# Kernel optimization log

Measured on AMD Instinct MI355X. Metric: run time of the kernel, lower is better.

## Reference

```python
import jax, jax.numpy as jnp
import numpy as np

N_EMBD = 1024
N_HEAD = 16
B, T = 2, 2048
LN_EPS = 1e-5


def _linear_params(key, d_in, d_out):
    k1, k2 = jax.random.split(key)
    bound = 1.0 / np.sqrt(d_in)
    W = jax.random.uniform(k1, (d_in, d_out), jnp.float32, -bound, bound)
    b = jax.random.uniform(k2, (d_out,), jnp.float32, -bound, bound)
    return W, b


def setup_inputs() -> dict:
    key = jax.random.key(0)
    ks = jax.random.split(key, 8)
    x = jax.random.normal(ks[0], (B, T, N_EMBD), jnp.float32)
    Wq, bq = _linear_params(ks[1], N_EMBD, N_EMBD)
    Wk, bk = _linear_params(ks[2], N_EMBD, N_EMBD)
    Wv, bv = _linear_params(ks[3], N_EMBD, N_EMBD)
    Wo, bo = _linear_params(ks[4], N_EMBD, N_EMBD)
    W1, b1 = _linear_params(ks[5], N_EMBD, 4 * N_EMBD)
    W2, b2 = _linear_params(ks[6], 4 * N_EMBD, N_EMBD)
    ln1_g = jnp.ones((N_EMBD,), jnp.float32)
    ln1_b = jnp.zeros((N_EMBD,), jnp.float32)
    ln2_g = jnp.ones((N_EMBD,), jnp.float32)
    ln2_b = jnp.zeros((N_EMBD,), jnp.float32)
    return dict(x=x, Wq=Wq, bq=bq, Wk=Wk, bk=bk, Wv=Wv, bv=bv, Wo=Wo, bo=bo,
                W1=W1, b1=b1, W2=W2, b2=b2,
                ln1_g=ln1_g, ln1_b=ln1_b, ln2_g=ln2_g, ln2_b=ln2_b)


def _layernorm(x, g, b):
    mu = jnp.mean(x, axis=-1, keepdims=True)
    var = jnp.mean(jnp.square(x - mu), axis=-1, keepdims=True)
    return (x - mu) * jax.lax.rsqrt(var + LN_EPS) * g + b


def _attention(x, Wq, bq, Wk, bk, Wv, bv, Wo, bo):
    Bsz, Tlen, C = x.shape
    hd = C // N_HEAD
    q = (x @ Wq + bq).reshape(Bsz, Tlen, N_HEAD, hd)
    k = (x @ Wk + bk).reshape(Bsz, Tlen, N_HEAD, hd)
    v = (x @ Wv + bv).reshape(Bsz, Tlen, N_HEAD, hd)
    scale = 1.0 / np.sqrt(hd)
    # NOTE: the original module's mask buffer is all ones -> masked_fill is a
    # no-op, so attention is FULL (non-causal) despite the class name.
    att = jnp.einsum('bqhd,bkhd->bhqk', q, k) * scale
    att = jax.nn.softmax(att, axis=-1)
    y = jnp.einsum('bhqk,bkhd->bqhd', att, v).reshape(Bsz, Tlen, C)
    return y @ Wo + bo


def reference(x, Wq, bq, Wk, bk, Wv, bv, Wo, bo, W1, b1, W2, b2,
              ln1_g, ln1_b, ln2_g, ln2_b):
    x = x + _attention(_layernorm(x, ln1_g, ln1_b), Wq, bq, Wk, bk, Wv, bv, Wo, bo)
    h = _layernorm(x, ln2_g, ln2_b)
    h = jax.nn.gelu(h @ W1 + b1, approximate=False) @ W2 + b2
    return x + h
```

## Files before the change

kernel.cpp:

```cpp
#include <hip/hip_runtime.h>
#include <hip/hip_bf16.h>
#include <math.h>


typedef __bf16 bf16x8 __attribute__((ext_vector_type(8)));
typedef float f32x4 __attribute__((ext_vector_type(4)));

__device__ __forceinline__ unsigned short f2bf(float f) {
  union { float f; unsigned int u; } v; v.f = f;
  unsigned int u = v.u;
  unsigned int r = (u + 0x7fffu + ((u >> 16) & 1u)) >> 16;
  return (unsigned short)r;
}

__device__ __forceinline__ unsigned int fbits(float f) {
  union { float f; unsigned int u; } v; v.f = f;
  return v.u;
}

__device__ __forceinline__ bf16x8 ld_bf16x8(const unsigned short* p) {
  union { uint4 u; bf16x8 v; } x;
  x.u = *(const uint4*)p;
  return x.v;
}

__device__ __forceinline__ float fast_exp2(float x) {
#if __has_builtin(__builtin_amdgcn_exp2f)
  return __builtin_amdgcn_exp2f(x);
#else
  return exp2f(x);
#endif
}

__device__ __forceinline__ size_t ckidx(int row, int col, int Kd) {
  return ((size_t)(row >> 4) * (Kd >> 5) + (col >> 5)) * 512 +
         (size_t)(((col >> 3) & 3) * 128 + (row & 15) * 8 + (col & 7));
}

__device__ __forceinline__ void async_copy16(const void* g, void* l) {
  __builtin_amdgcn_global_load_lds(
      (const __attribute__((address_space(1))) void*)g,
      (__attribute__((address_space(3))) void*)l, 16, 0, 0);
}

__global__ __launch_bounds__(256) void prep_kernel(
    const float* __restrict__ Wq, const float* __restrict__ Wk,
    const float* __restrict__ Wv, const float* __restrict__ Wo,
    const float* __restrict__ W1, const float* __restrict__ W2,
    unsigned short* __restrict__ WqT, unsigned short* __restrict__ WkT,
    unsigned short* __restrict__ WvT, unsigned short* __restrict__ WoT,
    unsigned short* __restrict__ W1T, unsigned short* __restrict__ W2T,
    const float* __restrict__ x, const float* __restrict__ g,
    const float* __restrict__ b, unsigned short* __restrict__ xn) {
  __shared__ unsigned short tile[32][33];
  __shared__ float red[8];
  const int id = blockIdx.x;
  const int t = threadIdx.x;

  if (id < 12288) {
    const float* W;
    unsigned short* Wt;
    int N, K, bx, by;
    if (id < 4096) {
      const int wsel = id >> 10, b10 = id & 1023;
      W = wsel == 0 ? Wq : (wsel == 1 ? Wk : (wsel == 2 ? Wv : Wo));
      Wt = wsel == 0 ? WqT : (wsel == 1 ? WkT : (wsel == 2 ? WvT : WoT));
      N = 1024; K = 1024; bx = b10 & 31; by = b10 >> 5;
    } else if (id < 8192) {
      const int b12 = id - 4096;
      W = W1; Wt = W1T; N = 4096; K = 1024; bx = b12 & 127; by = b12 >> 7;
    } else {
      const int b12 = id - 8192;
      W = W2; Wt = W2T; N = 1024; K = 4096; bx = b12 & 31; by = b12 >> 5;
    }
    const int n0 = bx * 32, k0 = by * 32;
    const int r = t >> 3, cq = (t & 7) * 4;
    float4 v = *(const float4*)&W[(size_t)(k0 + r) * N + n0 + cq];
    tile[cq + 0][r] = f2bf(v.x);
    tile[cq + 1][r] = f2bf(v.y);
    tile[cq + 2][r] = f2bf(v.z);
    tile[cq + 3][r] = f2bf(v.w);
    __syncthreads();
    ushort4 o;
    o.x = tile[r][cq + 0];
    o.y = tile[r][cq + 1];
    o.z = tile[r][cq + 2];
    o.w = tile[r][cq + 3];
    *(ushort4*)&Wt[ckidx(n0 + r, k0 + cq, K)] = o;
  } else {
    const int row = id - 12288;
    const float4 v = ((const float4*)(x + (size_t)row * 1024))[t];
    float s = v.x + v.y + v.z + v.w;
    float s2 = v.x * v.x + v.y * v.y + v.z * v.z + v.w * v.w;
    for (int o = 32; o > 0; o >>= 1) {
      s += __shfl_xor(s, o, 64);
      s2 += __shfl_xor(s2, o, 64);
    }
    const int w = t >> 6;
    if ((t & 63) == 0) { red[w] = s; red[4 + w] = s2; }
    __syncthreads();
    s = red[0] + red[1] + red[2] + red[3];
    s2 = red[4] + red[5] + red[6] + red[7];
    const float mu = s * (1.f / 1024.f);
    const float var = s2 * (1.f / 1024.f) - mu * mu;
    const float rs = rsqrtf(var + 1e-5f);
    const float4 gg = ((const float4*)g)[t];
    const float4 bb = ((const float4*)b)[t];
    ushort4 o4;
    o4.x = f2bf((v.x - mu) * rs * gg.x + bb.x);
    o4.y = f2bf((v.y - mu) * rs * gg.y + bb.y);
    o4.z = f2bf((v.z - mu) * rs * gg.z + bb.z);
    o4.w = f2bf((v.w - mu) * rs * gg.w + bb.w);
    *(ushort4*)&xn[ckidx(row, t * 4, 1024)] = o4;
  }
}

__global__ __launch_bounds__(256) void ln_kernel(
    const float* __restrict__ x, const float* __restrict__ g,
    const float* __restrict__ b, unsigned short* __restrict__ out) {
  const int row = blockIdx.x, t = threadIdx.x;
  const float4 v = ((const float4*)(x + (size_t)row * 1024))[t];
  float s = v.x + v.y + v.z + v.w;
  float s2 = v.x * v.x + v.y * v.y + v.z * v.z + v.w * v.w;
  for (int o = 32; o > 0; o >>= 1) {
    s += __shfl_xor(s, o, 64);
    s2 += __shfl_xor(s2, o, 64);
  }
  __shared__ float red[8];
  const int w = t >> 6;
  if ((t & 63) == 0) { red[w] = s; red[4 + w] = s2; }
  __syncthreads();
  s = red[0] + red[1] + red[2] + red[3];
  s2 = red[4] + red[5] + red[6] + red[7];
  const float mu = s * (1.f / 1024.f);
  const float var = s2 * (1.f / 1024.f) - mu * mu;
  const float rs = rsqrtf(var + 1e-5f);
  const float4 gg = ((const float4*)g)[t];
  const float4 bb = ((const float4*)b)[t];
  ushort4 o4;
  o4.x = f2bf((v.x - mu) * rs * gg.x + bb.x);
  o4.y = f2bf((v.y - mu) * rs * gg.y + bb.y);
  o4.z = f2bf((v.z - mu) * rs * gg.z + bb.z);
  o4.w = f2bf((v.w - mu) * rs * gg.w + bb.w);
  *(ushort4*)&out[ckidx(row, t * 4, 1024)] = o4;
}

enum { MODE_QKV = 0, MODE_RES = 1, MODE_GELU = 2 };

#define QSCALE 0.18033688011112043f

template <int MODE>
__global__ __launch_bounds__(512) void gemm256_kernel(
    const unsigned short* __restrict__ A, const unsigned short* __restrict__ Bt,
    const float* __restrict__ bias0, const float* __restrict__ bias1,
    const float* __restrict__ bias2,
    void* __restrict__ out0, void* __restrict__ out1, void* __restrict__ out2,
    int M, int N, int K) {
  __shared__ __align__(16) unsigned short L[2][64 * 512];
  const int t = threadIdx.x;
  const int l = t & 63, w = t >> 6;
  const int l8 = l * 8;
  const int lr = l & 15, lq = l >> 4;

  const int NT = N >> 8;
  const int q8 = (int)gridDim.x >> 3;
  const int bid = blockIdx.x;
  const int wg = (bid & 7) * q8 + (bid >> 3);
  const int mt = wg / NT, nt = wg % NT;
  const int m0 = mt << 8, n0 = nt << 8;

  const int ag0 = (w >> 2) * 8;
  const int bg0 = (w & 3) * 4;
  const int K32 = K >> 5;

  f32x4 acc[8][4];
#pragma unroll
  for (int i = 0; i < 8; i++)
#pragma unroll
    for (int j = 0; j < 4; j++) {
      f32x4 z = {0.f, 0.f, 0.f, 0.f};
      acc[i][j] = z;
    }

  auto issue = [&](int kt, int slot) {
    const int k32 = kt * 2;
#pragma unroll
    for (int j = 0; j < 8; j++) {
      const int c = j * 8 + w;
      unsigned short* dst = &L[slot][c * 512 + l8];
      if (j < 4) {
        const size_t cid =
            (size_t)((m0 >> 4) + (c & 15)) * K32 + (k32 + (c >> 4));
        async_copy16(&A[cid * 512 + l8], dst);
      } else {
        const int cb = c - 32;
        const size_t cid =
            (size_t)((n0 >> 4) + (cb & 15)) * K32 + (k32 + (cb >> 4));
        async_copy16(&Bt[cid * 512 + l8], dst);
      }
    }
  };

  const int KT = K >> 6;
  issue(0, 0);
  for (int kt = 0; kt < KT; kt++) {
    const int slot = kt & 1;
    if (kt + 1 < KT) {
      issue(kt + 1, slot ^ 1);
      asm volatile("s_waitcnt vmcnt(8)" ::: "memory");
    } else {
      asm volatile("s_waitcnt vmcnt(0)" ::: "memory");
    }
    __builtin_amdgcn_s_barrier();

    bf16x8 bfr[2][4];
#pragma unroll
    for (int kk = 0; kk < 2; kk++)
#pragma unroll
      for (int nj = 0; nj < 4; nj++)
        bfr[kk][nj] =
            ld_bf16x8(&L[slot][(32 + kk * 16 + bg0 + nj) * 512 + l8]);

#pragma unroll
    for (int half = 0; half < 2; half++) {
#pragma unroll
      for (int kk = 0; kk < 2; kk++) {
        bf16x8 afr[4];
#pragma unroll
        for (int mi = 0; mi < 4; mi++)
          afr[mi] = ld_bf16x8(
              &L[slot][(kk * 16 + ag0 + half * 4 + mi) * 512 + l8]);
        __builtin_amdgcn_s_setprio(1);
#pragma unroll
        for (int mi = 0; mi < 4; mi++)
#pragma unroll
          for (int nj = 0; nj < 4; nj++)
            acc[half * 4 + mi][nj] = __builtin_amdgcn_mfma_f32_16x16x32_bf16(
                afr[mi], bfr[kk][nj], acc[half * 4 + mi][nj], 0, 0, 0);
        __builtin_amdgcn_s_setprio(0);
      }
    }
    __builtin_amdgcn_s_barrier();
  }

#pragma unroll
  for (int mi8 = 0; mi8 < 8; mi8++) {
#pragma unroll
    for (int nj = 0; nj < 4; nj++) {
#pragma unroll
      for (int i = 0; i < 4; i++) {
        const int gm = m0 + (w >> 2) * 128 + mi8 * 16 + lq * 4 + i;
        const int gn = n0 + (w & 3) * 64 + nj * 16 + lr;
        const float v = acc[mi8][nj][i];
        if (MODE == MODE_QKV) {
          const int sel = gn >> 10, cn = gn & 1023;
          const int hh = cn >> 6, d = cn & 63;
          const int bb2 = gm >> 11, tok = gm & 2047;
          const size_t bh = (size_t)bb2 * 16 + hh;
          float u = v + (sel == 0 ? bias0 : (sel == 1 ? bias1 : bias2))[cn];
          if (sel == 0) {
            u *= QSCALE;
            const int qt = tok >> 7, r7 = tok & 127;
            const int ww = r7 >> 5, ss = (r7 >> 4) & 1, qlr = r7 & 15;
            const int kk = d >> 5, lq2 = (d >> 3) & 3, e = d & 7;
            const size_t idx =
                (((((bh * 16 + qt) * 4 + ww) * 2 + ss) * 2 + kk) << 9) +
                (lq2 * 16 + qlr) * 8 + e;
            ((unsigned short*)out0)[idx] = f2bf(u);
          } else if (sel == 1) {
            const int ktile = tok >> 6, r6 = tok & 63;
            const int nt2 = r6 >> 4, klr = r6 & 15;
            const int kk = d >> 5, lq2 = (d >> 3) & 3, e = d & 7;
            const size_t idx =
                ((((bh * 32 + ktile) * 4 + nt2) * 2 + kk) << 9) +
                (lq2 * 16 + klr) * 8 + e;
            ((unsigned short*)out1)[idx] = f2bf(u);
          } else {
            const int ktile = tok >> 6, r6 = tok & 63;
            const int kb = r6 >> 5, lq2 = (r6 >> 3) & 3, e = r6 & 7;
            const int nt2 = d >> 4, vlr = d & 15;
            const size_t idx =
                ((((bh * 32 + ktile) * 2 + kb) * 4 + nt2) << 9) +
                (lq2 * 16 + vlr) * 8 + e;
            ((unsigned short*)out2)[idx] = f2bf(u);
          }
        } else {
          const float u = v + bias0[gn];
          const float ge = 0.5f * u * (1.f + erff(u * 0.70710678118654752f));
          ((unsigned short*)out0)[ckidx(gm, gn, N)] = f2bf(ge);
        }
      }
    }
  }
}

template <int BM, int BN, int MODE>
__global__ __launch_bounds__(256) void gemm_kernel(
    const unsigned short* __restrict__ A, const unsigned short* __restrict__ Bt,
    const float* __restrict__ bias0, const float* __restrict__ residual,
    void* __restrict__ out0, int M, int N, int K) {
  constexpr int MI = BM / 32;
  constexpr int NI = BN / 32;
  constexpr int ACH = BM / 8;
  constexpr int BCH = BN / 8;
  __shared__ __align__(16) unsigned short As[2][BM * 64];
  __shared__ __align__(16) unsigned short Bs[2][BN * 64];
  const int t = threadIdx.x;

  const int NT = N / BN;
  const int NTX = NT >> 3;
  const int bid = blockIdx.x;
  const int xcd = bid & 7, local = bid >> 3;
  const int nt_ = xcd * NTX + local % NTX;
  const int mt = local / NTX;
  const int m0 = mt * BM, n0 = nt_ * BN;

  const int l = t & 63, w = t >> 6;
  const int l8 = l * 8;
  const int lr = l & 15, lq = l >> 4;
  const int K32 = K >> 5;

  f32x4 acc[MI][NI];
#pragma unroll
  for (int i = 0; i < MI; i++)
#pragma unroll
    for (int j = 0; j < NI; j++) {
      f32x4 z = {0.f, 0.f, 0.f, 0.f};
      acc[i][j] = z;
    }

  auto issue = [&](int k0, int p) {
    const int k32 = k0 >> 5;
#pragma unroll
    for (int j = 0; j < ACH / 4; j++) {
      const int c = j * 4 + w;
      const int g = c % (BM / 16), kk = c / (BM / 16);
      const size_t cid = (size_t)((m0 >> 4) + g) * K32 + (k32 + kk);
      async_copy16(&A[cid * 512 + l8], &As[p][c * 512 + l8]);
    }
#pragma unroll
    for (int j = 0; j < BCH / 4; j++) {
      const int c = j * 4 + w;
      const int g = c % (BN / 16), kk = c / (BN / 16);
      const size_t cid = (size_t)((n0 >> 4) + g) * K32 + (k32 + kk);
      async_copy16(&Bt[cid * 512 + l8], &Bs[p][c * 512 + l8]);
    }
  };

  issue(0, 0);
  int p = 0;
  for (int k0 = 0; k0 < K; k0 += 64) {
    __syncthreads();
    if (k0 + 64 < K) issue(k0 + 64, p ^ 1);
#pragma unroll
    for (int kk = 0; kk < 2; kk++) {
      bf16x8 af[MI], bf[NI];
#pragma unroll
      for (int mi = 0; mi < MI; mi++)
        af[mi] = ld_bf16x8(
            &As[p][(kk * (BM / 16) + (w >> 1) * (BM / 32) + mi) * 512 + l8]);
#pragma unroll
      for (int ni = 0; ni < NI; ni++)
        bf[ni] = ld_bf16x8(
            &Bs[p][(kk * (BN / 16) + (w & 1) * (BN / 32) + ni) * 512 + l8]);
#pragma unroll
      for (int mi = 0; mi < MI; mi++)
#pragma unroll
        for (int ni = 0; ni < NI; ni++)
          acc[mi][ni] = __builtin_amdgcn_mfma_f32_16x16x32_bf16(
              af[mi], bf[ni], acc[mi][ni], 0, 0, 0);
    }
    p ^= 1;
  }

  const int wm = (w >> 1) * (BM / 2), wn = (w & 1) * (BN / 2);
#pragma unroll
  for (int mi = 0; mi < MI; mi++) {
#pragma unroll
    for (int ni = 0; ni < NI; ni++) {
#pragma unroll
      for (int i = 0; i < 4; i++) {
        const int gm = m0 + wm + mi * 16 + lq * 4 + i;
        const int gn = n0 + wn + ni * 16 + lr;
        ((float*)out0)[(size_t)gm * N + gn] =
            acc[mi][ni][i] + bias0[gn] + residual[(size_t)gm * N + gn];
      }
    }
  }
}

__global__ __launch_bounds__(256) void attn_kernel(
    const unsigned short* __restrict__ Qp, const unsigned short* __restrict__ Kp,
    const unsigned short* __restrict__ Vp, unsigned short* __restrict__ O) {
  __shared__ __align__(16) unsigned short Ps[128 * 72];
  const int id = blockIdx.x;
  const int xcd = id & 7, loc = id >> 3;
  const int bh = xcd * 4 + (loc >> 4);
  const int qt = loc & 15;
  const int t = threadIdx.x, l = t & 63, w = t >> 6;
  const int lr = l & 15, lq = l >> 4;
  const int l8 = l * 8;
  const size_t rowBase = (size_t)(bh >> 4) * 2048;
  const int col0 = (bh & 15) * 64;

  const unsigned short* Qb_ = Qp + ((((size_t)bh * 16 + qt) * 4 + w) << 11);
  bf16x8 qf[2][2];
#pragma unroll
  for (int s = 0; s < 2; s++)
#pragma unroll
    for (int kk = 0; kk < 2; kk++)
      qf[s][kk] = ld_bf16x8(&Qb_[((s * 2 + kk) << 9) + l8]);

  const unsigned short* Kb_ = Kp + ((size_t)bh << 17);
  const unsigned short* Vb_ = Vp + ((size_t)bh << 17);

  bf16x8 kf[2][4];
#pragma unroll
  for (int nt = 0; nt < 4; nt++)
#pragma unroll
    for (int kk = 0; kk < 2; kk++)
      kf[kk][nt] = ld_bf16x8(&Kb_[((nt * 2 + kk) << 9) + l8]);

  f32x4 oacc[2][4];
#pragma unroll
  for (int s = 0; s < 2; s++)
#pragma unroll
    for (int nt = 0; nt < 4; nt++) {
      f32x4 z = {0.f, 0.f, 0.f, 0.f};
      oacc[s][nt] = z;
    }
  float lp[2] = {0.f, 0.f};

  for (int kt = 0; kt < 32; kt++) {
    const unsigned short* vtile = Vb_ + ((size_t)kt << 12);
    bf16x8 vf[2][4];
#pragma unroll
    for (int kb = 0; kb < 2; kb++)
#pragma unroll
      for (int nt = 0; nt < 4; nt++)
        vf[kb][nt] = ld_bf16x8(&vtile[((kb * 4 + nt) << 9) + l8]);

    f32x4 st[2][4];
#pragma unroll
    for (int s = 0; s < 2; s++)
#pragma unroll
      for (int nt = 0; nt < 4; nt++) {
        f32x4 z = {0.f, 0.f, 0.f, 0.f};
        st[s][nt] = z;
      }
#pragma unroll
    for (int nt = 0; nt < 4; nt++) {
      __builtin_amdgcn_s_setprio(1);
      st[0][nt] = __builtin_amdgcn_mfma_f32_16x16x32_bf16(kf[0][nt], qf[0][0], st[0][nt], 0, 0, 0);
      st[1][nt] = __builtin_amdgcn_mfma_f32_16x16x32_bf16(kf[0][nt], qf[1][0], st[1][nt], 0, 0, 0);
      st[0][nt] = __builtin_amdgcn_mfma_f32_16x16x32_bf16(kf[1][nt], qf[0][1], st[0][nt], 0, 0, 0);
      st[1][nt] = __builtin_amdgcn_mfma_f32_16x16x32_bf16(kf[1][nt], qf[1][1], st[1][nt], 0, 0, 0);
      __builtin_amdgcn_s_setprio(0);
    }

    const unsigned short* ktile_p = Kb_ + ((size_t)((kt + 1) & 31) << 12);
#pragma unroll
    for (int nt = 0; nt < 4; nt++)
#pragma unroll
      for (int kk = 0; kk < 2; kk++)
        kf[kk][nt] = ld_bf16x8(&ktile_p[((nt * 2 + kk) << 9) + l8]);

#pragma unroll
    for (int s = 0; s < 2; s++) {
      float rsum = 0.f;
#pragma unroll
      for (int nt = 0; nt < 4; nt++)
#pragma unroll
        for (int i = 0; i < 4; i++) {
          const float pv = fast_exp2(st[s][nt][i]);
          st[s][nt][i] = pv;
          rsum += pv;
        }
      lp[s] += rsum;
    }

#pragma unroll
    for (int s = 0; s < 2; s++)
#pragma unroll
      for (int nt = 0; nt < 4; nt++) {
        uint2 pk;
        pk.x = __builtin_amdgcn_perm(fbits(st[s][nt][1]), fbits(st[s][nt][0]), 0x07060302u);
        pk.y = __builtin_amdgcn_perm(fbits(st[s][nt][3]), fbits(st[s][nt][2]), 0x07060302u);
        *(uint2*)&Ps[(w * 32 + s * 16 + lr) * 72 + nt * 16 + lq * 4] = pk;
      }

#pragma unroll
    for (int kb = 0; kb < 2; kb++) {
      bf16x8 pf0 = ld_bf16x8(&Ps[(w * 32 + lr) * 72 + kb * 32 + lq * 8]);
      bf16x8 pf1 = ld_bf16x8(&Ps[(w * 32 + 16 + lr) * 72 + kb * 32 + lq * 8]);
      __builtin_amdgcn_s_setprio(1);
#pragma unroll
      for (int nt = 0; nt < 4; nt++) {
        oacc[0][nt] = __builtin_amdgcn_mfma_f32_16x16x32_bf16(pf0, vf[kb][nt], oacc[0][nt], 0, 0, 0);
        oacc[1][nt] = __builtin_amdgcn_mfma_f32_16x16x32_bf16(pf1, vf[kb][nt], oacc[1][nt], 0, 0, 0);
      }
      __builtin_amdgcn_s_setprio(0);
    }
  }

#pragma unroll
  for (int s = 0; s < 2; s++) {
    float li = lp[s];
    li += __shfl_xor(li, 16, 64);
    li += __shfl_xor(li, 32, 64);
    const float inv = 1.f / li;
#pragma unroll
    for (int nt = 0; nt < 4; nt++)
#pragma unroll
      for (int i = 0; i < 4; i++) {
        const int orow = (int)rowBase + qt * 128 + w * 32 + s * 16 + lq * 4 + i;
        const int ocol = col0 + nt * 16 + lr;
        O[ckidx(orow, ocol, 1024)] = f2bf(oacc[s][nt][i] * inv);
      }
  }
}

extern "C" void kernel_launch(void* const* d_in, const int* in_sizes, int n_in,
                              void* d_out, int out_size, void* d_ws, size_t ws_size,
                              hipStream_t stream) {
  const float* x    = (const float*)d_in[0];
  const float* Wq   = (const float*)d_in[1];
  const float* bq   = (const float*)d_in[2];
  const float* Wk   = (const float*)d_in[3];
  const float* bk   = (const float*)d_in[4];
  const float* Wv   = (const float*)d_in[5];
  const float* bv   = (const float*)d_in[6];
  const float* Wo   = (const float*)d_in[7];
  const float* bo   = (const float*)d_in[8];
  const float* W1   = (const float*)d_in[9];
  const float* b1   = (const float*)d_in[10];
  const float* W2   = (const float*)d_in[11];
  const float* b2   = (const float*)d_in[12];
  const float* ln1g = (const float*)d_in[13];
  const float* ln1b = (const float*)d_in[14];
  const float* ln2g = (const float*)d_in[15];
  const float* ln2b = (const float*)d_in[16];

  char* ws = (char*)d_ws;
  const size_t MB = 1024ull * 1024ull;
  unsigned short* WqT = (unsigned short*)(ws + 0 * MB);
  unsigned short* WkT = (unsigned short*)(ws + 2 * MB);
  unsigned short* WvT = (unsigned short*)(ws + 4 * MB);
  unsigned short* WoT = (unsigned short*)(ws + 6 * MB);
  unsigned short* W1T = (unsigned short*)(ws + 8 * MB);
  unsigned short* W2T = (unsigned short*)(ws + 16 * MB);
  unsigned short* xn  = (unsigned short*)(ws + 24 * MB);
  unsigned short* Qp  = (unsigned short*)(ws + 32 * MB);
  unsigned short* Kp  = (unsigned short*)(ws + 40 * MB);
  unsigned short* Vp  = (unsigned short*)(ws + 48 * MB);
  unsigned short* Ob  = (unsigned short*)(ws + 56 * MB);
  float*          x1  = (float*)(ws + 64 * MB);
  unsigned short* h2  = (unsigned short*)(ws + 80 * MB);
  unsigned short* Hb  = (unsigned short*)(ws + 24 * MB);

  const dim3 blk(256);
  const dim3 blk512(512);

  prep_kernel<<<dim3(16384), blk, 0, stream>>>(
      Wq, Wk, Wv, Wo, W1, W2, WqT, WkT, WvT, WoT, W1T, W2T,
      x, ln1g, ln1b, xn);

  gemm256_kernel<MODE_QKV><<<dim3(192), blk512, 0, stream>>>(
      xn, WqT, bq, bk, bv, Qp, Kp, Vp, 4096, 3072, 1024);

  attn_kernel<<<dim3(512), blk, 0, stream>>>(Qp, Kp, Vp, Ob);

  gemm_kernel<64, 128, MODE_RES><<<dim3(8 * 64), blk, 0, stream>>>(
      Ob, WoT, bo, x, x1, 4096, 1024, 1024);

  ln_kernel<<<4096, blk, 0, stream>>>(x1, ln2g, ln2b, h2);

  gemm256_kernel<MODE_GELU><<<dim3(256), blk512, 0, stream>>>(
      h2, W1T, b1, nullptr, nullptr, Hb, nullptr, nullptr, 4096, 4096, 1024);

  gemm_kernel<64, 128, MODE_RES><<<dim3(8 * 64), blk, 0, stream>>>(
      Hb, W2T, b2, x1, (float*)d_out, 4096, 1024, 4096);
}
```

Baseline: 365.1 us.

## Replace 64x128 residual GEMM with 128x128 tile, 512-thread pipelined kernel

The templated 64x128/256-thread residual GEMM used for the output projection and the second MLP matmul is replaced by a dedicated 128x128 tile kernel with 8 waves. Each wave now computes a 64x32 sub-tile. A single shared buffer is double-buffered and synchronised with explicit vmcnt waits and raw barriers, so loads for the next tile overlap compute. MFMA sections are wrapped in raised wave priority. Larger tiles improve data reuse but halve the grid to 256 blocks, which may lower occupancy on a 256-CU device.

```diff
diff --git a/kernel.cpp b/kernel.cpp
--- a/kernel.cpp
+++ b/kernel.cpp
@@ -294,96 +294,103 @@
   }
 }
 
-template <int BM, int BN, int MODE>
-__global__ __launch_bounds__(256) void gemm_kernel(
+__global__ __launch_bounds__(512) void gemm128_kernel(
     const unsigned short* __restrict__ A, const unsigned short* __restrict__ Bt,
     const float* __restrict__ bias0, const float* __restrict__ residual,
-    void* __restrict__ out0, int M, int N, int K) {
-  constexpr int MI = BM / 32;
-  constexpr int NI = BN / 32;
-  constexpr int ACH = BM / 8;
-  constexpr int BCH = BN / 8;
-  __shared__ __align__(16) unsigned short As[2][BM * 64];
-  __shared__ __align__(16) unsigned short Bs[2][BN * 64];
+    float* __restrict__ out0, int M, int N, int K) {
+  __shared__ __align__(16) unsigned short L[2][32 * 512];
   const int t = threadIdx.x;
-
-  const int NT = N / BN;
-  const int NTX = NT >> 3;
-  const int bid = blockIdx.x;
-  const int xcd = bid & 7, local = bid >> 3;
-  const int nt_ = xcd * NTX + local % NTX;
-  const int mt = local / NTX;
-  const int m0 = mt * BM, n0 = nt_ * BN;
-
   const int l = t & 63, w = t >> 6;
   const int l8 = l * 8;
   const int lr = l & 15, lq = l >> 4;
+
+  const int NT = N >> 7;
+  const int q8 = (int)gridDim.x >> 3;
+  const int bid = blockIdx.x;
+  const int wg = (bid & 7) * q8 + (bid >> 3);
+  const int mt = wg / NT, nt = wg % NT;
+  const int m0 = mt << 7, n0 = nt << 7;
+
+  const int ag0 = (w >> 2) * 4;
+  const int bg0 = (w & 3) * 2;
   const int K32 = K >> 5;
 
-  f32x4 acc[MI][NI];
-#pragma unroll
-  for (int i = 0; i < MI; i++)
-#pragma unroll
-    for (int j = 0; j < NI; j++) {
+  f32x4 acc[4][2];
+#pragma unroll
+  for (int i = 0; i < 4; i++)
+#pragma unroll
+    for (int j = 0; j < 2; j++) {
       f32x4 z = {0.f, 0.f, 0.f, 0.f};
       acc[i][j] = z;
     }
 
-  auto issue = [&](int k0, int p) {
-    const int k32 = k0 >> 5;
-#pragma unroll
-    for (int j = 0; j < ACH / 4; j++) {
-      const int c = j * 4 + w;
-      const int g = c % (BM / 16), kk = c / (BM / 16);
-      const size_t cid = (size_t)((m0 >> 4) + g) * K32 + (k32 + kk);
-      async_copy16(&A[cid * 512 + l8], &As[p][c * 512 + l8]);
-    }
-#pragma unroll
-    for (int j = 0; j < BCH / 4; j++) {
-      const int c = j * 4 + w;
-      const int g = c % (BN / 16), kk = c / (BN / 16);
-      const size_t cid = (size_t)((n0 >> 4) + g) * K32 + (k32 + kk);
-      async_copy16(&Bt[cid * 512 + l8], &Bs[p][c * 512 + l8]);
+  auto issue = [&](int kt, int slot) {
+    const int k32 = kt * 2;
+#pragma unroll
+    for (int j = 0; j < 4; j++) {
+      const int c = j * 8 + w;
+      unsigned short* dst = &L[slot][c * 512 + l8];
+      if (j < 2) {
+        const size_t cid =
+            (size_t)((m0 >> 4) + (c & 7)) * K32 + (k32 + (c >> 3));
+        async_copy16(&A[cid * 512 + l8], dst);
+      } else {
+        const int cb = c - 16;
+        const size_t cid =
+            (size_t)((n0 >> 4) + (cb & 7)) * K32 + (k32 + (cb >> 3));
+        async_copy16(&Bt[cid * 512 + l8], dst);
+      }
     }
   };
 
+  const int KT = K >> 6;
   issue(0, 0);
-  int p = 0;
-  for (int k0 = 0; k0 < K; k0 += 64) {
-    __syncthreads();
-    if (k0 + 64 < K) issue(k0 + 64, p ^ 1);
+  for (int kt = 0; kt < KT; kt++) {
+    const int slot = kt & 1;
+    if (kt + 1 < KT) {
+      issue(kt + 1, slot ^ 1);
+      asm volatile("s_waitcnt vmcnt(4)" ::: "memory");
+    } else {
+      asm volatile("s_waitcnt vmcnt(0)" ::: "memory");
+    }
+    __builtin_amdgcn_s_barrier();
+
+    bf16x8 bfr[2][2];
+#pragma unroll
+    for (int kk = 0; kk < 2; kk++)
+#pragma unroll
+      for (int nj = 0; nj < 2; nj++)
+        bfr[kk][nj] =
+            ld_bf16x8(&L[slot][(16 + kk * 8 + bg0 + nj) * 512 + l8]);
+
 #pragma unroll
     for (int kk = 0; kk < 2; kk++) {
-      bf16x8 af[MI], bf[NI];
-#pragma unroll
-      for (int mi = 0; mi < MI; mi++)
-        af[mi] = ld_bf16x8(
-            &As[p][(kk * (BM / 16) + (w >> 1) * (BM / 32) + mi) * 512 + l8]);
-#pragma unroll
-      for (int ni = 0; ni < NI; ni++)
-        bf[ni] = ld_bf16x8(
-            &Bs[p][(kk * (BN / 16) + (w & 1) * (BN / 32) + ni) * 512 + l8]);
-#pragma unroll
-      for (int mi = 0; mi < MI; mi++)
-#pragma unroll
-        for (int ni = 0; ni < NI; ni++)
-          acc[mi][ni] = __builtin_amdgcn_mfma_f32_16x16x32_bf16(
-              af[mi], bf[ni], acc[mi][ni], 0, 0, 0);
-    }
-    p ^= 1;
-  }
-
-  const int wm = (w >> 1) * (BM / 2), wn = (w & 1) * (BN / 2);
-#pragma unroll
-  for (int mi = 0; mi < MI; mi++) {
-#pragma unroll
-    for (int ni = 0; ni < NI; ni++) {
+      bf16x8 afr[4];
+#pragma unroll
+      for (int mi = 0; mi < 4; mi++)
+        afr[mi] = ld_bf16x8(&L[slot][(kk * 8 + ag0 + mi) * 512 + l8]);
+      __builtin_amdgcn_s_setprio(1);
+#pragma unroll
+      for (int mi = 0; mi < 4; mi++)
+#pragma unroll
+        for (int nj = 0; nj < 2; nj++)
+          acc[mi][nj] = __builtin_amdgcn_mfma_f32_16x16x32_bf16(
+              afr[mi], bfr[kk][nj], acc[mi][nj], 0, 0, 0);
+      __builtin_amdgcn_s_setprio(0);
+    }
+    __builtin_amdgcn_s_barrier();
+  }
+
+#pragma unroll
+  for (int mi = 0; mi < 4; mi++) {
+#pragma unroll
+    for (int nj = 0; nj < 2; nj++) {
 #pragma unroll
       for (int i = 0; i < 4; i++) {
-        const int gm = m0 + wm + mi * 16 + lq * 4 + i;
-        const int gn = n0 + wn + ni * 16 + lr;
-        ((float*)out0)[(size_t)gm * N + gn] =
-            acc[mi][ni][i] + bias0[gn] + residual[(size_t)gm * N + gn];
+        const int gm = m0 + (w >> 2) * 64 + mi * 16 + lq * 4 + i;
+        const int gn = n0 + (w & 3) * 32 + nj * 16 + lr;
+        out0[(size_t)gm * N + gn] =
+            acc[mi][nj][i] + bias0[gn] + residual[(size_t)gm * N + gn];
       }
     }
   }
@@ -570,7 +577,7 @@
 
   attn_kernel<<<dim3(512), blk, 0, stream>>>(Qp, Kp, Vp, Ob);
 
-  gemm_kernel<64, 128, MODE_RES><<<dim3(8 * 64), blk, 0, stream>>>(
+  gemm128_kernel<<<dim3(256), blk512, 0, stream>>>(
       Ob, WoT, bo, x, x1, 4096, 1024, 1024);
 
   ln_kernel<<<4096, blk, 0, stream>>>(x1, ln2g, ln2b, h2);
@@ -578,6 +585,6 @@
   gemm256_kernel<MODE_GELU><<<dim3(256), blk512, 0, stream>>>(
       h2, W1T, b1, nullptr, nullptr, Hb, nullptr, nullptr, 4096, 4096, 1024);
 
-  gemm_kernel<64, 128, MODE_RES><<<dim3(8 * 64), blk, 0, stream>>>(
+  gemm128_kernel<<<dim3(256), blk512, 0, stream>>>(
       Hb, W2T, b2, x1, (float*)d_out, 4096, 1024, 4096);
 }
```

New measurement: 447.5 us. +22.5%, slower.
